# Kernel tuning notes

Measured on AMD Instinct MI355X. Metric: run time of the kernel, lower is better.

## Reference

```python
import jax, jax.numpy as jnp
import numpy as np

BATCH = 4096
TEMP = 0.5
EPS = 1e-12  # torch F.normalize eps

def setup_inputs() -> dict:
    key = jax.random.key(0)
    k1, k2 = jax.random.split(key)
    z_i = jax.random.normal(k1, (BATCH, 256), dtype=jnp.float32)
    z_j = jax.random.normal(k2, (BATCH, 256), dtype=jnp.float32)
    return {"z_i": z_i, "z_j": z_j}

def _l2norm(x):
    n = jnp.sqrt(jnp.sum(x * x, axis=1, keepdims=True))
    return x / jnp.maximum(n, EPS)

def reference(z_i, z_j):
    B = z_i.shape[0]
    zi = _l2norm(z_i)
    zj = _l2norm(z_j)
    reps = jnp.concatenate([zi, zj], axis=0)          # [2B, D]
    # rows are unit-norm, so cosine similarity == dot product (GEMM)
    sim = reps @ reps.T                                # [2B, 2B]
    sim_ij = jnp.diagonal(sim, offset=B)               # [B]
    sim_ji = jnp.diagonal(sim, offset=-B)              # [B]
    positives = jnp.concatenate([sim_ij, sim_ji], 0)   # [2B]
    nominator = jnp.exp(positives / TEMP)
    # negatives_mask: ones with the two same-view BxB diagonal blocks zeroed
    idx = jnp.arange(2 * B)
    half = (idx >= B).astype(sim.dtype)                # 0 for first half, 1 for second
    mask = (half[:, None] != half[None, :]).astype(sim.dtype)  # cross-view blocks = 1
    denom = jnp.sum(mask * jnp.exp(sim / TEMP), axis=1)
    loss_partial = -jnp.log(nominator / denom)
    return jnp.sum(loss_partial) / (2 * B)
```

## Files before the change

### kernel.cpp

```cpp
#include <hip/hip_runtime.h>
#include <hip/hip_bf16.h>

#define BATCH 4096
#define DIM 256

typedef __attribute__((ext_vector_type(8))) short short8;
typedef __attribute__((ext_vector_type(4))) float f32x4;

__device__ inline unsigned short f2bf(float f) {
    union { float f; unsigned u; } x; x.f = f;
    unsigned r = x.u + 0x7fffu + ((x.u >> 16) & 1u);
    return (unsigned short)(r >> 16);
}

#define WS_FAST_BYTES ((size_t)4 * 1024 * 1024 + 3 * 4096 * sizeof(float))

__device__ inline short8* lds8(unsigned short* base, int r, int c) {
    int byte = (r << 7) + (c << 1);
    byte ^= (r & 7) << 4;
    return reinterpret_cast<short8*>(reinterpret_cast<char*>(base) + byte);
}

__global__ __launch_bounds__(256) void norm2_kernel(
    const float* __restrict__ zi, const float* __restrict__ zj,
    unsigned short* __restrict__ zib, unsigned short* __restrict__ zjb,
    float* __restrict__ pos, float* __restrict__ rowsum, float* __restrict__ colsum) {
    const int tid = threadIdx.x;
    if (blockIdx.x < 16) rowsum[blockIdx.x * 256 + tid] = 0.f;
    else if (blockIdx.x < 32) colsum[(blockIdx.x - 16) * 256 + tid] = 0.f;

    const int wid  = tid >> 6;
    const int lane = tid & 63;
    const int row  = blockIdx.x * 4 + wid;
    const float4 vi = reinterpret_cast<const float4*>(zi)[row * 64 + lane];
    const float4 vj = reinterpret_cast<const float4*>(zj)[row * 64 + lane];
    float si = vi.x * vi.x + vi.y * vi.y + vi.z * vi.z + vi.w * vi.w;
    float sj = vj.x * vj.x + vj.y * vj.y + vj.z * vj.z + vj.w * vj.w;
    float d  = vi.x * vj.x + vi.y * vj.y + vi.z * vj.z + vi.w * vj.w;
#pragma unroll
    for (int o = 1; o < 64; o <<= 1) {
        si += __shfl_xor(si, o);
        sj += __shfl_xor(sj, o);
        d  += __shfl_xor(d, o);
    }
    const float ii = 1.0f / fmaxf(sqrtf(si), 1e-12f);
    const float ij = 1.0f / fmaxf(sqrtf(sj), 1e-12f);
    ushort4 a = make_ushort4(f2bf(vi.x * ii), f2bf(vi.y * ii), f2bf(vi.z * ii), f2bf(vi.w * ii));
    ushort4 b = make_ushort4(f2bf(vj.x * ij), f2bf(vj.y * ij), f2bf(vj.z * ij), f2bf(vj.w * ij));
    reinterpret_cast<ushort4*>(zib)[row * 64 + lane] = a;
    reinterpret_cast<ushort4*>(zjb)[row * 64 + lane] = b;
    if (lane == 0) pos[row] = d * ii * ij;
}

__global__ __launch_bounds__(256) void sim128_kernel(
    const unsigned short* __restrict__ zib, const unsigned short* __restrict__ zjb,
    float* __restrict__ rowsum, float* __restrict__ colsum) {
    __shared__ unsigned short As[128 * 64];
    __shared__ unsigned short Bs[128 * 64];
    const int bi = blockIdx.x, bj = blockIdx.y;
    const int tid  = threadIdx.x;
    const int wave = tid >> 6;
    const int lane = tid & 63;
    const int wr = (wave >> 1) << 6;
    const int wc = (wave & 1) << 6;
    const int fr = lane & 15;
    const int ko = (lane >> 4) << 3;

    f32x4 acc[4][4] = {};

    for (int s = 0; s < 4; ++s) {
        if (s) __syncthreads();
#pragma unroll
        for (int i = 0; i < 4; ++i) {
            int chunk = i * 256 + tid;
            int r = chunk >> 3;
            int c16 = chunk & 7;
            const short8 va = *reinterpret_cast<const short8*>(
                zib + (size_t)(bi * 128 + r) * DIM + s * 64 + c16 * 8);
            const short8 vb = *reinterpret_cast<const short8*>(
                zjb + (size_t)(bj * 128 + r) * DIM + s * 64 + c16 * 8);
            *lds8(As, r, c16 * 8) = va;
            *lds8(Bs, r, c16 * 8) = vb;
        }
        __syncthreads();
#pragma unroll
        for (int kk = 0; kk < 2; ++kk) {
            int c = kk * 32 + ko;
            short8 a0 = *lds8(As, wr +      fr, c);
            short8 a1 = *lds8(As, wr + 16 + fr, c);
            short8 a2 = *lds8(As, wr + 32 + fr, c);
            short8 a3 = *lds8(As, wr + 48 + fr, c);
            short8 b0 = *lds8(Bs, wc +      fr, c);
            short8 b1 = *lds8(Bs, wc + 16 + fr, c);
            short8 b2 = *lds8(Bs, wc + 32 + fr, c);
            short8 b3 = *lds8(Bs, wc + 48 + fr, c);
            acc[0][0] = __builtin_amdgcn_mfma_f32_16x16x32_bf16(a0, b0, acc[0][0], 0, 0, 0);
            acc[0][1] = __builtin_amdgcn_mfma_f32_16x16x32_bf16(a0, b1, acc[0][1], 0, 0, 0);
            acc[0][2] = __builtin_amdgcn_mfma_f32_16x16x32_bf16(a0, b2, acc[0][2], 0, 0, 0);
            acc[0][3] = __builtin_amdgcn_mfma_f32_16x16x32_bf16(a0, b3, acc[0][3], 0, 0, 0);
            acc[1][0] = __builtin_amdgcn_mfma_f32_16x16x32_bf16(a1, b0, acc[1][0], 0, 0, 0);
            acc[1][1] = __builtin_amdgcn_mfma_f32_16x16x32_bf16(a1, b1, acc[1][1], 0, 0, 0);
            acc[1][2] = __builtin_amdgcn_mfma_f32_16x16x32_bf16(a1, b2, acc[1][2], 0, 0, 0);
            acc[1][3] = __builtin_amdgcn_mfma_f32_16x16x32_bf16(a1, b3, acc[1][3], 0, 0, 0);
            acc[2][0] = __builtin_amdgcn_mfma_f32_16x16x32_bf16(a2, b0, acc[2][0], 0, 0, 0);
            acc[2][1] = __builtin_amdgcn_mfma_f32_16x16x32_bf16(a2, b1, acc[2][1], 0, 0, 0);
            acc[2][2] = __builtin_amdgcn_mfma_f32_16x16x32_bf16(a2, b2, acc[2][2], 0, 0, 0);
            acc[2][3] = __builtin_amdgcn_mfma_f32_16x16x32_bf16(a2, b3, acc[2][3], 0, 0, 0);
            acc[3][0] = __builtin_amdgcn_mfma_f32_16x16x32_bf16(a3, b0, acc[3][0], 0, 0, 0);
            acc[3][1] = __builtin_amdgcn_mfma_f32_16x16x32_bf16(a3, b1, acc[3][1], 0, 0, 0);
            acc[3][2] = __builtin_amdgcn_mfma_f32_16x16x32_bf16(a3, b2, acc[3][2], 0, 0, 0);
            acc[3][3] = __builtin_amdgcn_mfma_f32_16x16x32_bf16(a3, b3, acc[3][3], 0, 0, 0);
        }
    }

    const float SC = 2.0f * 1.44269504088896f;
    float rs[4][4];
#pragma unroll
    for (int m = 0; m < 4; ++m)
#pragma unroll
        for (int r = 0; r < 4; ++r) rs[m][r] = 0.f;
    float cs[4] = {0.f, 0.f, 0.f, 0.f};
#pragma unroll
    for (int m = 0; m < 4; ++m)
#pragma unroll
        for (int n = 0; n < 4; ++n)
#pragma unroll
            for (int r = 0; r < 4; ++r) {
                float e = exp2f(acc[m][n][r] * SC);
                rs[m][r] += e;
                cs[n] += e;
            }

#pragma unroll
    for (int m = 0; m < 4; ++m)
#pragma unroll
        for (int r = 0; r < 4; ++r) {
            float v = rs[m][r];
            v += __shfl_xor(v, 1); v += __shfl_xor(v, 2);
            v += __shfl_xor(v, 4); v += __shfl_xor(v, 8);
            if ((lane & 15) == 0) {
                int row = bi * 128 + wr + m * 16 + (lane >> 4) * 4 + r;
                atomicAdd(&rowsum[row], v);
            }
        }
#pragma unroll
    for (int n = 0; n < 4; ++n) {
        float v = cs[n];
        v += __shfl_xor(v, 16); v += __shfl_xor(v, 32);
        if (lane < 16) atomicAdd(&colsum[bj * 128 + wc + n * 16 + lane], v);
    }
}

__global__ __launch_bounds__(256) void loss_kernel(
    const float* __restrict__ rowsum, const float* __restrict__ colsum,
    const float* __restrict__ pos, float* __restrict__ out) {
    float a = 0.f;
    for (int i = threadIdx.x; i < BATCH; i += 256)
        a += __logf(rowsum[i]) + __logf(colsum[i]) - 4.0f * pos[i];
#pragma unroll
    for (int o = 1; o < 64; o <<= 1) a += __shfl_xor(a, o);
    __shared__ float red[4];
    if ((threadIdx.x & 63) == 0) red[threadIdx.x >> 6] = a;
    __syncthreads();
    if (threadIdx.x == 0) {
        float t = red[0] + red[1] + red[2] + red[3];
        out[0] = t * (1.0f / (2.0f * BATCH));
    }
}

__device__ inline short8* ldsp128(unsigned short* base, int r, int c) {
    int byte = (r << 8) + (c << 1);
    byte ^= (r & 7) << 4;
    return reinterpret_cast<short8*>(reinterpret_cast<char*>(base) + byte);
}

__global__ __launch_bounds__(256) void init_kernel(float* __restrict__ rowsum,
                                                   float* __restrict__ colsum) {
    int i = blockIdx.x * 256 + threadIdx.x;
    rowsum[i] = 0.f;
    colsum[i] = 0.f;
}

__global__ __launch_bounds__(256) void norm_kernel(
    const float* __restrict__ zi, const float* __restrict__ zj,
    float* __restrict__ ninv_i, float* __restrict__ ninv_j, float* __restrict__ pos) {
    const int wid  = threadIdx.x >> 6;
    const int lane = threadIdx.x & 63;
    const int row  = blockIdx.x * 4 + wid;
    const float4 vi = reinterpret_cast<const float4*>(zi)[row * 64 + lane];
    const float4 vj = reinterpret_cast<const float4*>(zj)[row * 64 + lane];
    float si = vi.x * vi.x + vi.y * vi.y + vi.z * vi.z + vi.w * vi.w;
    float sj = vj.x * vj.x + vj.y * vj.y + vj.z * vj.z + vj.w * vj.w;
    float d  = vi.x * vj.x + vi.y * vj.y + vi.z * vj.z + vi.w * vj.w;
#pragma unroll
    for (int o = 1; o < 64; o <<= 1) {
        si += __shfl_xor(si, o);
        sj += __shfl_xor(sj, o);
        d  += __shfl_xor(d, o);
    }
    if (lane == 0) {
        float ii = 1.0f / fmaxf(sqrtf(si), 1e-12f);
        float ij = 1.0f / fmaxf(sqrtf(sj), 1e-12f);
        ninv_i[row] = ii;
        ninv_j[row] = ij;
        pos[row] = d * ii * ij;
    }
}

__global__ __launch_bounds__(256) void sim_kernel(
    const float* __restrict__ zi, const float* __restrict__ zj,
    const float* __restrict__ ninv_i, const float* __restrict__ ninv_j,
    float* __restrict__ rowsum, float* __restrict__ colsum) {
    __shared__ unsigned short As[64 * 128];
    __shared__ unsigned short Bs[64 * 128];
    const int bi = blockIdx.x, bj = blockIdx.y;
    const int tid  = threadIdx.x;
    const int wave = tid >> 6;
    const int lane = tid & 63;
    const int wr = (wave >> 1) << 5;
    const int wc = (wave & 1) << 5;
    const int fr = lane & 15;
    const int ko = (lane >> 4) << 3;

    f32x4 acc[2][2] = {};

    for (int h = 0; h < 2; ++h) {
#pragma unroll
        for (int it = 0; it < 4; ++it) {
            int chunk = tid + it * 256;
            int r = chunk >> 4;
            int c = (chunk & 15) << 3;
            int ga = bi * 64 + r;
            int gb = bj * 64 + r;
            int cg = h * 128 + c;
            const float4* pa = reinterpret_cast<const float4*>(zi) + ga * 64 + (cg >> 2);
            const float4* pb = reinterpret_cast<const float4*>(zj) + gb * 64 + (cg >> 2);
            float4 a0 = pa[0], a1 = pa[1];
            float4 b0 = pb[0], b1 = pb[1];
            float ia = ninv_i[ga];
            float ib = ninv_j[gb];
            short8 va, vb;
            va[0] = (short)f2bf(a0.x * ia); va[1] = (short)f2bf(a0.y * ia);
            va[2] = (short)f2bf(a0.z * ia); va[3] = (short)f2bf(a0.w * ia);
            va[4] = (short)f2bf(a1.x * ia); va[5] = (short)f2bf(a1.y * ia);
            va[6] = (short)f2bf(a1.z * ia); va[7] = (short)f2bf(a1.w * ia);
            vb[0] = (short)f2bf(b0.x * ib); vb[1] = (short)f2bf(b0.y * ib);
            vb[2] = (short)f2bf(b0.z * ib); vb[3] = (short)f2bf(b0.w * ib);
            vb[4] = (short)f2bf(b1.x * ib); vb[5] = (short)f2bf(b1.y * ib);
            vb[6] = (short)f2bf(b1.z * ib); vb[7] = (short)f2bf(b1.w * ib);
            *ldsp128(As, r, c) = va;
            *ldsp128(Bs, r, c) = vb;
        }
        __syncthreads();
#pragma unroll
        for (int kk = 0; kk < 4; ++kk) {
            int c = kk * 32 + ko;
            short8 a0 = *ldsp128(As, wr + fr, c);
            short8 a1 = *ldsp128(As, wr + 16 + fr, c);
            short8 b0 = *ldsp128(Bs, wc + fr, c);
            short8 b1 = *ldsp128(Bs, wc + 16 + fr, c);
            acc[0][0] = __builtin_amdgcn_mfma_f32_16x16x32_bf16(a0, b0, acc[0][0], 0, 0, 0);
            acc[0][1] = __builtin_amdgcn_mfma_f32_16x16x32_bf16(a0, b1, acc[0][1], 0, 0, 0);
            acc[1][0] = __builtin_amdgcn_mfma_f32_16x16x32_bf16(a1, b0, acc[1][0], 0, 0, 0);
            acc[1][1] = __builtin_amdgcn_mfma_f32_16x16x32_bf16(a1, b1, acc[1][1], 0, 0, 0);
        }
        __syncthreads();
    }

    const float SC = 2.0f * 1.44269504088896f;
    float rs[2][4];
#pragma unroll
    for (int m = 0; m < 2; ++m)
#pragma unroll
        for (int r = 0; r < 4; ++r) rs[m][r] = 0.f;
    float cs[2] = {0.f, 0.f};
#pragma unroll
    for (int m = 0; m < 2; ++m)
#pragma unroll
        for (int n = 0; n < 2; ++n)
#pragma unroll
            for (int r = 0; r < 4; ++r) {
                float e = exp2f(acc[m][n][r] * SC);
                rs[m][r] += e;
                cs[n] += e;
            }
#pragma unroll
    for (int m = 0; m < 2; ++m)
#pragma unroll
        for (int r = 0; r < 4; ++r) {
            float v = rs[m][r];
            v += __shfl_xor(v, 1); v += __shfl_xor(v, 2);
            v += __shfl_xor(v, 4); v += __shfl_xor(v, 8);
            if ((lane & 15) == 0) {
                int row = bi * 64 + wr + m * 16 + (lane >> 4) * 4 + r;
                atomicAdd(&rowsum[row], v);
            }
        }
#pragma unroll
    for (int n = 0; n < 2; ++n) {
        float v = cs[n];
        v += __shfl_xor(v, 16); v += __shfl_xor(v, 32);
        if (lane < 16) atomicAdd(&colsum[bj * 64 + wc + n * 16 + lane], v);
    }
}

extern "C" void kernel_launch(void* const* d_in, const int* in_sizes, int n_in,
                              void* d_out, int out_size, void* d_ws, size_t ws_size,
                              hipStream_t stream) {
    const float* zi = (const float*)d_in[0];
    const float* zj = (const float*)d_in[1];
    char* ws = (char*)d_ws;

    if (ws_size >= WS_FAST_BYTES) {
        unsigned short* zib = (unsigned short*)ws;
        unsigned short* zjb = (unsigned short*)(ws + (size_t)2 * 1024 * 1024);
        float* pos    = (float*)(ws + (size_t)4 * 1024 * 1024);
        float* rowsum = pos + 4096;
        float* colsum = rowsum + 4096;
        norm2_kernel<<<BATCH / 4, 256, 0, stream>>>(zi, zj, zib, zjb, pos, rowsum, colsum);
        dim3 grid(32, 32);
        sim128_kernel<<<grid, 256, 0, stream>>>(zib, zjb, rowsum, colsum);
        loss_kernel<<<1, 256, 0, stream>>>(rowsum, colsum, pos, (float*)d_out);
    } else {
        float* wsf = (float*)ws;
        float* ninv_i = wsf;
        float* ninv_j = wsf + 4096;
        float* pos    = wsf + 8192;
        float* rowsum = wsf + 12288;
        float* colsum = wsf + 16384;
        init_kernel<<<16, 256, 0, stream>>>(rowsum, colsum);
        norm_kernel<<<BATCH / 4, 256, 0, stream>>>(zi, zj, ninv_i, ninv_j, pos);
        dim3 grid(64, 64);
        sim_kernel<<<grid, 256, 0, stream>>>(zi, zj, ninv_i, ninv_j, rowsum, colsum);
        loss_kernel<<<1, 256, 0, stream>>>(rowsum, colsum, pos, (float*)d_out);
    }
}
```

Measured before the change: 37.30 us.

## Use direct global-to-LDS loads and fuse final loss into GEMM via last-block ticket

The bf16 tile loads in the similarity kernel now use global_load_lds, so data goes straight into shared memory without a register round trip. The swizzle is kept by permuting which global column each lane fetches. The separate single-block loss kernel is removed: each GEMM block bumps an atomic ticket, and the last block to finish computes the log-sum reduction and writes the output. This saves one kernel launch and the register staging cost, but adds a threadfence and an atomic per block, and the final reduction runs serially in a single block.

```diff
diff --git a/kernel.cpp b/kernel.cpp
--- a/kernel.cpp
+++ b/kernel.cpp
@@ -13,7 +13,13 @@
     return (unsigned short)(r >> 16);
 }
 
-#define WS_FAST_BYTES ((size_t)4 * 1024 * 1024 + 3 * 4096 * sizeof(float))
+__device__ __forceinline__ void gload16(const void* g, void* l) {
+    __builtin_amdgcn_global_load_lds(
+        (const __attribute__((address_space(1))) unsigned int*)g,
+        (__attribute__((address_space(3))) unsigned int*)l, 16, 0, 0);
+}
+
+#define WS_FAST_BYTES ((size_t)4 * 1024 * 1024 + 3 * 4096 * sizeof(float) + 64)
 
 __device__ inline short8* lds8(unsigned short* base, int r, int c) {
     int byte = (r << 7) + (c << 1);
@@ -24,10 +30,12 @@
 __global__ __launch_bounds__(256) void norm2_kernel(
     const float* __restrict__ zi, const float* __restrict__ zj,
     unsigned short* __restrict__ zib, unsigned short* __restrict__ zjb,
-    float* __restrict__ pos, float* __restrict__ rowsum, float* __restrict__ colsum) {
+    float* __restrict__ pos, float* __restrict__ rowsum, float* __restrict__ colsum,
+    int* __restrict__ counter) {
     const int tid = threadIdx.x;
     if (blockIdx.x < 16) rowsum[blockIdx.x * 256 + tid] = 0.f;
     else if (blockIdx.x < 32) colsum[(blockIdx.x - 16) * 256 + tid] = 0.f;
+    if (blockIdx.x == 32 && tid == 0) *counter = 0;
 
     const int wid  = tid >> 6;
     const int lane = tid & 63;
@@ -54,7 +62,9 @@
 
 __global__ __launch_bounds__(256) void sim128_kernel(
     const unsigned short* __restrict__ zib, const unsigned short* __restrict__ zjb,
-    float* __restrict__ rowsum, float* __restrict__ colsum) {
+    float* __restrict__ rowsum, float* __restrict__ colsum,
+    const float* __restrict__ pos, int* __restrict__ counter,
+    float* __restrict__ out) {
     __shared__ unsigned short As[128 * 64];
     __shared__ unsigned short Bs[128 * 64];
     const int bi = blockIdx.x, bj = blockIdx.y;
@@ -66,21 +76,21 @@
     const int fr = lane & 15;
     const int ko = (lane >> 4) << 3;
 
+    const int l8 = lane >> 3;
+    const int cg = (lane & 7) ^ l8;
+    const int srow = wave << 5;
+
     f32x4 acc[4][4] = {};
 
     for (int s = 0; s < 4; ++s) {
         if (s) __syncthreads();
 #pragma unroll
-        for (int i = 0; i < 4; ++i) {
-            int chunk = i * 256 + tid;
-            int r = chunk >> 3;
-            int c16 = chunk & 7;
-            const short8 va = *reinterpret_cast<const short8*>(
-                zib + (size_t)(bi * 128 + r) * DIM + s * 64 + c16 * 8);
-            const short8 vb = *reinterpret_cast<const short8*>(
-                zjb + (size_t)(bj * 128 + r) * DIM + s * 64 + c16 * 8);
-            *lds8(As, r, c16 * 8) = va;
-            *lds8(Bs, r, c16 * 8) = vb;
+        for (int t = 0; t < 4; ++t) {
+            const int r = srow + t * 8 + l8;
+            const unsigned short* ga = zib + (size_t)(bi * 128 + r) * DIM + s * 64 + cg * 8;
+            const unsigned short* gb = zjb + (size_t)(bj * 128 + r) * DIM + s * 64 + cg * 8;
+            gload16(ga, (char*)As + (srow + t * 8) * 128);
+            gload16(gb, (char*)Bs + (srow + t * 8) * 128);
         }
         __syncthreads();
 #pragma unroll
@@ -149,6 +159,26 @@
         v += __shfl_xor(v, 16); v += __shfl_xor(v, 32);
         if (lane < 16) atomicAdd(&colsum[bj * 128 + wc + n * 16 + lane], v);
     }
+
+    __threadfence();
+    int* sticket = (int*)Bs;
+    if (tid == 0) *sticket = atomicAdd(counter, 1);
+    __syncthreads();
+    if (*sticket == 1023) {
+        __threadfence();
+        float a = 0.f;
+        for (int i = tid; i < BATCH; i += 256)
+            a += __logf(rowsum[i]) + __logf(colsum[i]) - 4.0f * pos[i];
+#pragma unroll
+        for (int o = 1; o < 64; o <<= 1) a += __shfl_xor(a, o);
+        float* red = (float*)As;
+        if ((tid & 63) == 0) red[tid >> 6] = a;
+        __syncthreads();
+        if (tid == 0) {
+            float t = red[0] + red[1] + red[2] + red[3];
+            out[0] = t * (1.0f / (2.0f * BATCH));
+        }
+    }
 }
 
 __global__ __launch_bounds__(256) void loss_kernel(
@@ -232,9 +262,9 @@
             int c = (chunk & 15) << 3;
             int ga = bi * 64 + r;
             int gb = bj * 64 + r;
-            int cg = h * 128 + c;
-            const float4* pa = reinterpret_cast<const float4*>(zi) + ga * 64 + (cg >> 2);
-            const float4* pb = reinterpret_cast<const float4*>(zj) + gb * 64 + (cg >> 2);
+            int cgl = h * 128 + c;
+            const float4* pa = reinterpret_cast<const float4*>(zi) + ga * 64 + (cgl >> 2);
+            const float4* pb = reinterpret_cast<const float4*>(zj) + gb * 64 + (cgl >> 2);
             float4 a0 = pa[0], a1 = pa[1];
             float4 b0 = pb[0], b1 = pb[1];
             float ia = ninv_i[ga];
@@ -317,10 +347,10 @@
         float* pos    = (float*)(ws + (size_t)4 * 1024 * 1024);
         float* rowsum = pos + 4096;
         float* colsum = rowsum + 4096;
-        norm2_kernel<<<BATCH / 4, 256, 0, stream>>>(zi, zj, zib, zjb, pos, rowsum, colsum);
+        int*   counter = (int*)(colsum + 4096);
+        norm2_kernel<<<BATCH / 4, 256, 0, stream>>>(zi, zj, zib, zjb, pos, rowsum, colsum, counter);
         dim3 grid(32, 32);
-        sim128_kernel<<<grid, 256, 0, stream>>>(zib, zjb, rowsum, colsum);
-        loss_kernel<<<1, 256, 0, stream>>>(rowsum, colsum, pos, (float*)d_out);
+        sim128_kernel<<<grid, 256, 0, stream>>>(zib, zjb, rowsum, colsum, pos, counter, (float*)d_out);
     } else {
         float* wsf = (float*)ws;
         float* ninv_i = wsf;
```

Result: slower. 91.31 us (+144.8%).

## Double-buffer LDS tiles in sim128 kernel to overlap global loads with MFMA

Applied to the files above, without the earlier changes.

Converts the sim128 GEMM main loop to a register-staged, double-buffered LDS pipeline. The next K-slice is loaded from global memory into registers before the MFMAs on the current buffer, then written to the other buffer, which drops one barrier per iteration. The aim is to hide global load latency behind compute. In exchange it doubles LDS use to 64 KB per block, which may lower occupancy, and adds register pressure. A variable rename in another kernel and the extra 64 bytes of workspace padding are incidental.

```diff
diff --git a/kernel.cpp b/kernel.cpp
--- a/kernel.cpp
+++ b/kernel.cpp
@@ -13,7 +13,7 @@
     return (unsigned short)(r >> 16);
 }
 
-#define WS_FAST_BYTES ((size_t)4 * 1024 * 1024 + 3 * 4096 * sizeof(float))
+#define WS_FAST_BYTES ((size_t)4 * 1024 * 1024 + 3 * 4096 * sizeof(float) + 64)
 
 __device__ inline short8* lds8(unsigned short* base, int r, int c) {
     int byte = (r << 7) + (c << 1);
@@ -55,8 +55,8 @@
 __global__ __launch_bounds__(256) void sim128_kernel(
     const unsigned short* __restrict__ zib, const unsigned short* __restrict__ zjb,
     float* __restrict__ rowsum, float* __restrict__ colsum) {
-    __shared__ unsigned short As[128 * 64];
-    __shared__ unsigned short Bs[128 * 64];
+    __shared__ unsigned short As[2][128 * 64];
+    __shared__ unsigned short Bs[2][128 * 64];
     const int bi = blockIdx.x, bj = blockIdx.y;
     const int tid  = threadIdx.x;
     const int wave = tid >> 6;
@@ -66,34 +66,52 @@
     const int fr = lane & 15;
     const int ko = (lane >> 4) << 3;
 
+    const unsigned short* gA = zib + (size_t)bi * 128 * DIM;
+    const unsigned short* gB = zjb + (size_t)bj * 128 * DIM;
+    int rr[4], cc[4];
+#pragma unroll
+    for (int i = 0; i < 4; ++i) {
+        int chunk = i * 256 + tid;
+        rr[i] = chunk >> 3;
+        cc[i] = (chunk & 7) << 3;
+    }
+
+    short8 pa[4], pb[4];
+#pragma unroll
+    for (int i = 0; i < 4; ++i) {
+        pa[i] = *reinterpret_cast<const short8*>(gA + rr[i] * DIM + cc[i]);
+        pb[i] = *reinterpret_cast<const short8*>(gB + rr[i] * DIM + cc[i]);
+    }
+#pragma unroll
+    for (int i = 0; i < 4; ++i) {
+        *lds8(As[0], rr[i], cc[i]) = pa[i];
+        *lds8(Bs[0], rr[i], cc[i]) = pb[i];
+    }
+
     f32x4 acc[4][4] = {};
 
+#pragma unroll
     for (int s = 0; s < 4; ++s) {
-        if (s) __syncthreads();
-#pragma unroll
-        for (int i = 0; i < 4; ++i) {
-            int chunk = i * 256 + tid;
-            int r = chunk >> 3;
-            int c16 = chunk & 7;
-            const short8 va = *reinterpret_cast<const short8*>(
-                zib + (size_t)(bi * 128 + r) * DIM + s * 64 + c16 * 8);
-            const short8 vb = *reinterpret_cast<const short8*>(
-                zjb + (size_t)(bj * 128 + r) * DIM + s * 64 + c16 * 8);
-            *lds8(As, r, c16 * 8) = va;
-            *lds8(Bs, r, c16 * 8) = vb;
-        }
+        const int cur = s & 1;
         __syncthreads();
+        if (s < 3) {
+#pragma unroll
+            for (int i = 0; i < 4; ++i) {
+                pa[i] = *reinterpret_cast<const short8*>(gA + rr[i] * DIM + (s + 1) * 64 + cc[i]);
+                pb[i] = *reinterpret_cast<const short8*>(gB + rr[i] * DIM + (s + 1) * 64 + cc[i]);
+            }
+        }
 #pragma unroll
         for (int kk = 0; kk < 2; ++kk) {
             int c = kk * 32 + ko;
-            short8 a0 = *lds8(As, wr +      fr, c);
-            short8 a1 = *lds8(As, wr + 16 + fr, c);
-            short8 a2 = *lds8(As, wr + 32 + fr, c);
-            short8 a3 = *lds8(As, wr + 48 + fr, c);
-            short8 b0 = *lds8(Bs, wc +      fr, c);
-            short8 b1 = *lds8(Bs, wc + 16 + fr, c);
-            short8 b2 = *lds8(Bs, wc + 32 + fr, c);
-            short8 b3 = *lds8(Bs, wc + 48 + fr, c);
+            short8 a0 = *lds8(As[cur], wr +      fr, c);
+            short8 a1 = *lds8(As[cur], wr + 16 + fr, c);
+            short8 a2 = *lds8(As[cur], wr + 32 + fr, c);
+            short8 a3 = *lds8(As[cur], wr + 48 + fr, c);
+            short8 b0 = *lds8(Bs[cur], wc +      fr, c);
+            short8 b1 = *lds8(Bs[cur], wc + 16 + fr, c);
+            short8 b2 = *lds8(Bs[cur], wc + 32 + fr, c);
+            short8 b3 = *lds8(Bs[cur], wc + 48 + fr, c);
             acc[0][0] = __builtin_amdgcn_mfma_f32_16x16x32_bf16(a0, b0, acc[0][0], 0, 0, 0);
             acc[0][1] = __builtin_amdgcn_mfma_f32_16x16x32_bf16(a0, b1, acc[0][1], 0, 0, 0);
             acc[0][2] = __builtin_amdgcn_mfma_f32_16x16x32_bf16(a0, b2, acc[0][2], 0, 0, 0);
@@ -111,6 +129,13 @@
             acc[3][2] = __builtin_amdgcn_mfma_f32_16x16x32_bf16(a3, b2, acc[3][2], 0, 0, 0);
             acc[3][3] = __builtin_amdgcn_mfma_f32_16x16x32_bf16(a3, b3, acc[3][3], 0, 0, 0);
         }
+        if (s < 3) {
+#pragma unroll
+            for (int i = 0; i < 4; ++i) {
+                *lds8(As[cur ^ 1], rr[i], cc[i]) = pa[i];
+                *lds8(Bs[cur ^ 1], rr[i], cc[i]) = pb[i];
+            }
+        }
     }
 
     const float SC = 2.0f * 1.44269504088896f;
@@ -232,9 +257,9 @@
             int c = (chunk & 15) << 3;
             int ga = bi * 64 + r;
             int gb = bj * 64 + r;
-            int cg = h * 128 + c;
-            const float4* pa = reinterpret_cast<const float4*>(zi) + ga * 64 + (cg >> 2);
-            const float4* pb = reinterpret_cast<const float4*>(zj) + gb * 64 + (cg >> 2);
+            int cgl = h * 128 + c;
+            const float4* pa = reinterpret_cast<const float4*>(zi) + ga * 64 + (cgl >> 2);
+            const float4* pb = reinterpret_cast<const float4*>(zj) + gb * 64 + (cgl >> 2);
             float4 a0 = pa[0], a1 = pa[1];
             float4 b0 = pb[0], b1 = pb[1];
             float ia = ninv_i[ga];
```

After: 36.67 us. Within noise of the previous version (-1.7%).
